# Kernel optimization log

Hardware: AMD Instinct MI355X
Metric: run time of the kernel (lower is better)

The kernel has to match this reference:

```python
import jax, jax.numpy as jnp
import numpy as np

B, M = 2048, 128

def _linear_params(key, out_dim, in_dim):
    k1, k2 = jax.random.split(key)
    bound = 1.0 / np.sqrt(in_dim)
    w = jax.random.uniform(k1, (out_dim, in_dim), jnp.float32, -bound, bound)
    b = jax.random.uniform(k2, (out_dim,), jnp.float32, -bound, bound)
    return w, b

def setup_inputs() -> dict:
    key = jax.random.key(0)
    ks = jax.random.split(key, 11)
    dyn = jax.random.normal(ks[0], (B, M, 3), jnp.float32)
    static = jax.random.normal(ks[1], (B, 3), jnp.float32)
    phi_w1, phi_b1 = _linear_params(ks[2], 120, 3)
    phi_w2, phi_b2 = _linear_params(ks[3], 100, 120)
    phi_w3, phi_b3 = _linear_params(ks[4], 80, 100)
    rho_w1, rho_b1 = _linear_params(ks[5], 60, 80)
    rho_w2, rho_b2 = _linear_params(ks[6], 60, 60)
    rho_w3, rho_b3 = _linear_params(ks[7], 40, 60)
    q_w1, q_b1 = _linear_params(ks[8], 200, 43)
    q_w2, q_b2 = _linear_params(ks[9], 100, 200)
    q_w3, q_b3 = _linear_params(ks[10], 3, 100)
    return dict(dyn=dyn, static=static,
                phi_w1=phi_w1, phi_b1=phi_b1, phi_w2=phi_w2, phi_b2=phi_b2,
                phi_w3=phi_w3, phi_b3=phi_b3,
                rho_w1=rho_w1, rho_b1=rho_b1, rho_w2=rho_w2, rho_b2=rho_b2,
                rho_w3=rho_w3, rho_b3=rho_b3,
                q_w1=q_w1, q_b1=q_b1, q_w2=q_w2, q_b2=q_b2, q_w3=q_w3, q_b3=q_b3)

def reference(dyn, static,
              phi_w1, phi_b1, phi_w2, phi_b2, phi_w3, phi_b3,
              rho_w1, rho_b1, rho_w2, rho_b2, rho_w3, rho_b3,
              q_w1, q_b1, q_w2, q_b2, q_w3, q_b3):
    relu = jax.nn.relu
    # Phi: per-element 3-layer MLP (all layers ReLU), then sum-pool over elements.
    h = relu(jnp.einsum('bmi,oi->bmo', dyn, phi_w1) + phi_b1)   # [B,M,120]
    h = relu(jnp.einsum('bmi,oi->bmo', h, phi_w2) + phi_b2)     # [B,M,100]
    h = relu(jnp.einsum('bmi,oi->bmo', h, phi_w3) + phi_b3)     # [B,M,80]
    pooled = h.sum(axis=1)                                       # [B,80] segment-sum
    # Rho: 80 -> 40 (no activation on last layer)
    r = relu(pooled @ rho_w1.T + rho_b1)
    r = relu(r @ rho_w2.T + rho_b2)
    r = r @ rho_w3.T + rho_b3                                    # [B,40]
    x = jnp.concatenate([r, static], axis=1)                     # [B,43]
    # Q head: 43 -> 3 with softmax
    q = relu(x @ q_w1.T + q_b1)
    q = relu(q @ q_w2.T + q_b2)
    q = q @ q_w3.T + q_b3
    return jax.nn.softmax(q, axis=1)                             # [B,3]
```

## Files before the change

### kernel.cpp

```cpp
#include <hip/hip_runtime.h>
#include <math.h>

typedef short s16x8 __attribute__((ext_vector_type(8)));
typedef short s16x4 __attribute__((ext_vector_type(4)));
typedef float f32x4 __attribute__((ext_vector_type(4)));

__device__ __forceinline__ void bsplit(float x, short& hi, short& lo) {
    unsigned u  = __float_as_uint(x);
    unsigned uh = u & 0xFFFF0000u;
    hi = (short)(uh >> 16);
    float r = x - __uint_as_float(uh);
    lo = (short)(__float_as_uint(r) >> 16);
}

#define MFMA_B16(A, B, C) __builtin_amdgcn_mfma_f32_16x16x32_bf16((A), (B), (C), 0, 0, 0)

__global__ __launch_bounds__(512, 4)
void ds_all(const float* __restrict__ dyn, const float* __restrict__ stat,
            const float* __restrict__ pw1, const float* __restrict__ pb1,
            const float* __restrict__ pw2, const float* __restrict__ pb2,
            const float* __restrict__ pw3, const float* __restrict__ pb3,
            const float* __restrict__ rw1, const float* __restrict__ rb1,
            const float* __restrict__ rw2, const float* __restrict__ rb2,
            const float* __restrict__ rw3, const float* __restrict__ rb3,
            const float* __restrict__ qw1, const float* __restrict__ qb1,
            const float* __restrict__ qw2, const float* __restrict__ qb2,
            const float* __restrict__ qw3, const float* __restrict__ qb3,
            float* __restrict__ out) {
    const int tid = threadIdx.x;
    const int w = tid >> 6, l = tid & 63, ln = l & 15, l4 = l >> 4;
    const int b = blockIdx.x;

    __shared__ __align__(16) float xs[384];
    __shared__ short h1H[2048], h1L[2048];
    __shared__ short h2H[2048], h2L[2048];
    __shared__ __align__(16) float pooledS[80];
    __shared__ __align__(16) float r1s[64], r2s[64], xcat[48], q1s[200], q2s[104];
    __shared__ float logits[3];

    if (tid < 96)
        *(f32x4*)(xs + tid * 4) = *(const f32x4*)(dyn + (size_t)b * 384 + tid * 4);

    if (tid < 128) {
        const int t = tid & 63, row = t >> 2, q = t & 3;
        const int col = (112 + q * 4) ^ ((row & 7) << 3);
        s16x4 z = 0;
        short* dst = (tid < 64) ? h2H : h2L;
        *(s16x4*)(dst + row * 128 + col) = z;
    }

    const int grow = tid >> 5;
    const int k0   = (tid & 31) * 4;
    f32x4 c1_0, c1_1, c1_2, c1_3;
    #define LDC(J, C) do { const int k = k0 + (J);                              \
        if (k < 120) { C.x = pw1[k*3]; C.y = pw1[k*3+1]; C.z = pw1[k*3+2];      \
                       C.w = pb1[k]; }                                          \
        else C = 0.f; } while (0)
    LDC(0, c1_0); LDC(1, c1_1); LDC(2, c1_2); LDC(3, c1_3);
    #undef LDC

    const int arow = 16 * w + ln;
    s16x8 w2h0=0,w2h1=0,w2h2=0,w2h3=0, w2l0=0,w2l1=0,w2l2=0,w2l3=0;
    s16x8 w3h0=0,w3h1=0,w3h2=0,w3h3=0, w3l0=0,w3l1=0,w3l2=0,w3l3=0;
    f32x4 bb2 = 0.f, bb3 = 0.f;
    if (w < 7) {
        #define LDW2(KS, DH, DL) do { s16x8 vh, vl;                             \
            _Pragma("unroll")                                                   \
            for (int j = 0; j < 8; ++j) {                                       \
                const int c = (KS) * 32 + l4 * 8 + j;                           \
                float v = (arow < 100 && c < 120) ? pw2[arow * 120 + c] : 0.f;  \
                short hi, lo; bsplit(v, hi, lo); vh[j] = hi; vl[j] = lo;        \
            } DH = vh; DL = vl; } while (0)
        LDW2(0, w2h0, w2l0); LDW2(1, w2h1, w2l1);
        LDW2(2, w2h2, w2l2); LDW2(3, w2h3, w2l3);
        #undef LDW2
        const int o0 = 16 * w + 4 * l4;
        #pragma unroll
        for (int r = 0; r < 4; ++r) bb2[r] = (o0 + r < 100) ? pb2[o0 + r] : 0.f;
    }
    if (w < 5) {
        #define LDW3(KS, DH, DL) do { s16x8 vh, vl;                             \
            _Pragma("unroll")                                                   \
            for (int j = 0; j < 8; ++j) {                                       \
                const int c = (KS) * 32 + l4 * 8 + j;                           \
                float v = (c < 100) ? pw3[arow * 100 + c] : 0.f;                \
                short hi, lo; bsplit(v, hi, lo); vh[j] = hi; vl[j] = lo;        \
            } DH = vh; DL = vl; } while (0)
        LDW3(0, w3h0, w3l0); LDW3(1, w3h1, w3l1);
        LDW3(2, w3h2, w3l2); LDW3(3, w3h3, w3l3);
        #undef LDW3
        bb3 = *(const f32x4*)(pb3 + 16 * w + 4 * l4);
    }
    __syncthreads();

    float pool0 = 0.f, pool1 = 0.f, pool2 = 0.f, pool3 = 0.f;
    const int swzR = (ln & 7) << 3;
    const int swzG = (grow & 7) << 3;

    #pragma unroll 1
    for (int T = 0; T < 8; ++T) {
        {
            const int el = 16 * T + grow;
            const float x0 = xs[el * 3], x1 = xs[el * 3 + 1], x2 = xs[el * 3 + 2];
            s16x4 vh, vl;
            #define GEN(J, C) do {                                              \
                float v = fmaf(x0, C.x, fmaf(x1, C.y, fmaf(x2, C.z, C.w)));     \
                v = fmaxf(v, 0.f);                                              \
                short hi, lo; bsplit(v, hi, lo); vh[J] = hi; vl[J] = lo;        \
            } while (0)
            GEN(0, c1_0); GEN(1, c1_1); GEN(2, c1_2); GEN(3, c1_3);
            #undef GEN
            const int idx = grow * 128 + (k0 ^ swzG);
            *(s16x4*)(h1H + idx) = vh;
            *(s16x4*)(h1L + idx) = vl;
        }
        __syncthreads();

        if (w < 7) {
            f32x4 a2h = 0.f, a2x = 0.f;
            #define L2K(KS, WH, WL) do {                                        \
                const int bidx = ln * 128 + (((KS) * 32 + l4 * 8) ^ swzR);      \
                const s16x8 bh = *(const s16x8*)(h1H + bidx);                   \
                const s16x8 bl = *(const s16x8*)(h1L + bidx);                   \
                a2h = MFMA_B16(WH, bh, a2h);                                    \
                a2x = MFMA_B16(WH, bl, a2x);                                    \
                a2x = MFMA_B16(WL, bh, a2x);                                    \
            } while (0)
            L2K(0, w2h0, w2l0); L2K(1, w2h1, w2l1);
            L2K(2, w2h2, w2l2); L2K(3, w2h3, w2l3);
            #undef L2K
            s16x4 oh, ol;
            #pragma unroll
            for (int r = 0; r < 4; ++r) {
                float v = fmaxf(a2h[r] + a2x[r] + bb2[r], 0.f);
                short hi, lo; bsplit(v, hi, lo);
                oh[r] = hi; ol[r] = lo;
            }
            const int idx2 = ln * 128 + ((16 * w + 4 * l4) ^ swzR);
            *(s16x4*)(h2H + idx2) = oh;
            *(s16x4*)(h2L + idx2) = ol;
        }
        __syncthreads();

        if (w < 5) {
            f32x4 a3 = 0.f, a3x = 0.f;
            #define L3K(KS, WH, WL) do {                                        \
                const int bidx = ln * 128 + (((KS) * 32 + l4 * 8) ^ swzR);      \
                const s16x8 bh = *(const s16x8*)(h2H + bidx);                   \
                const s16x8 bl = *(const s16x8*)(h2L + bidx);                   \
                a3  = MFMA_B16(WH, bh, a3);                                     \
                a3x = MFMA_B16(WH, bl, a3x);                                    \
                a3x = MFMA_B16(WL, bh, a3x);                                    \
            } while (0)
            L3K(0, w3h0, w3l0); L3K(1, w3h1, w3l1);
            L3K(2, w3h2, w3l2); L3K(3, w3h3, w3l3);
            #undef L3K
            pool0 += fmaxf(a3[0] + a3x[0] + bb3[0], 0.f);
            pool1 += fmaxf(a3[1] + a3x[1] + bb3[1], 0.f);
            pool2 += fmaxf(a3[2] + a3x[2] + bb3[2], 0.f);
            pool3 += fmaxf(a3[3] + a3x[3] + bb3[3], 0.f);
        }
        __syncthreads();
    }

    if (w < 5) {
        #pragma unroll
        for (int d = 1; d < 16; d <<= 1) {
            pool0 += __shfl_xor(pool0, d);
            pool1 += __shfl_xor(pool1, d);
            pool2 += __shfl_xor(pool2, d);
            pool3 += __shfl_xor(pool3, d);
        }
        if (ln == 0) {
            const int o0 = 16 * w + 4 * l4;
            pooledS[o0 + 0] = pool0;
            pooledS[o0 + 1] = pool1;
            pooledS[o0 + 2] = pool2;
            pooledS[o0 + 3] = pool3;
        }
    }
    __syncthreads();

    if (tid < 60) {
        float a = rb1[tid];
        for (int k = 0; k < 80; k += 4) {
            f32x4 pv = *(const f32x4*)(pooledS + k);
            f32x4 wv = *(const f32x4*)(rw1 + tid * 80 + k);
            a += pv.x * wv.x + pv.y * wv.y + pv.z * wv.z + pv.w * wv.w;
        }
        r1s[tid] = fmaxf(a, 0.0f);
    }
    __syncthreads();
    if (tid < 60) {
        float a = rb2[tid];
        for (int k = 0; k < 60; k += 4) {
            f32x4 pv = *(const f32x4*)(r1s + k);
            f32x4 wv = *(const f32x4*)(rw2 + tid * 60 + k);
            a += pv.x * wv.x + pv.y * wv.y + pv.z * wv.z + pv.w * wv.w;
        }
        r2s[tid] = fmaxf(a, 0.0f);
    }
    __syncthreads();
    if (tid < 40) {
        float a = rb3[tid];
        for (int k = 0; k < 60; k += 4) {
            f32x4 pv = *(const f32x4*)(r2s + k);
            f32x4 wv = *(const f32x4*)(rw3 + tid * 60 + k);
            a += pv.x * wv.x + pv.y * wv.y + pv.z * wv.z + pv.w * wv.w;
        }
        xcat[tid] = a;
    }
    if (tid >= 40 && tid < 43) xcat[tid] = stat[(size_t)b * 3 + (tid - 40)];
    __syncthreads();
    if (tid < 200) {
        float a = qb1[tid];
        const float* wv = qw1 + tid * 43;
        for (int k = 0; k < 43; ++k) a += xcat[k] * wv[k];
        q1s[tid] = fmaxf(a, 0.0f);
    }
    __syncthreads();
    if (tid < 100) {
        float a = qb2[tid];
        for (int k = 0; k < 200; k += 4) {
            f32x4 pv = *(const f32x4*)(q1s + k);
            f32x4 wv = *(const f32x4*)(qw2 + tid * 200 + k);
            a += pv.x * wv.x + pv.y * wv.y + pv.z * wv.z + pv.w * wv.w;
        }
        q2s[tid] = fmaxf(a, 0.0f);
    }
    __syncthreads();
    if (tid < 96) {
        int o = tid >> 5, l2 = tid & 31;
        float a = 0.0f;
        for (int k = l2; k < 100; k += 32) a += q2s[k] * qw3[o * 100 + k];
        #pragma unroll
        for (int d = 16; d > 0; d >>= 1) a += __shfl_down(a, d, 32);
        if (l2 == 0) logits[o] = a + qb3[o];
    }
    __syncthreads();
    if (tid < 3) {
        float l0 = logits[0], l1 = logits[1], l2v = logits[2];
        float m  = fmaxf(l0, fmaxf(l1, l2v));
        float e0 = __expf(l0 - m), e1 = __expf(l1 - m), e2 = __expf(l2v - m);
        float inv = 1.0f / (e0 + e1 + e2);
        float mine = (tid == 0) ? e0 : ((tid == 1) ? e1 : e2);
        out[(size_t)b * 3 + tid] = mine * inv;
    }
}

extern "C" void kernel_launch(void* const* d_in, const int* in_sizes, int n_in,
                              void* d_out, int out_size, void* d_ws, size_t ws_size,
                              hipStream_t stream) {
    const float* dyn  = (const float*)d_in[0];
    const float* stat = (const float*)d_in[1];
    const float* pw1  = (const float*)d_in[2];
    const float* pb1  = (const float*)d_in[3];
    const float* pw2  = (const float*)d_in[4];
    const float* pb2  = (const float*)d_in[5];
    const float* pw3  = (const float*)d_in[6];
    const float* pb3  = (const float*)d_in[7];
    const float* rw1  = (const float*)d_in[8];
    const float* rb1  = (const float*)d_in[9];
    const float* rw2  = (const float*)d_in[10];
    const float* rb2  = (const float*)d_in[11];
    const float* rw3  = (const float*)d_in[12];
    const float* rb3  = (const float*)d_in[13];
    const float* qw1  = (const float*)d_in[14];
    const float* qb1  = (const float*)d_in[15];
    const float* qw2  = (const float*)d_in[16];
    const float* qb2  = (const float*)d_in[17];
    const float* qw3  = (const float*)d_in[18];
    const float* qb3  = (const float*)d_in[19];
    float* out = (float*)d_out;

    const int B = in_sizes[0] / 384;
    ds_all<<<dim3(B), dim3(512), 0, stream>>>(dyn, stat,
        pw1, pb1, pw2, pb2, pw3, pb3,
        rw1, rb1, rw2, rb2, rw3, rb3,
        qw1, qb1, qw2, qb2, qw3, qb3, out);
}
```

Before: 190.6 us.

## Split MFMA accumulator chains, raise priority, and parallelize the rho/Q head dot-products

Each phi-layer MFMA sequence now uses three independent accumulators instead of two, shortening the dependent chain. Shared-memory fragment loads are batched two k-steps at a time, and the MFMA region runs at raised wave priority via s_setprio. The serial per-output dot products in the rho and Q-head tail now split each reduction across 2 or 4 lanes, combined with shuffles. The aim is less latency on the per-batch serial tail and in the MFMA chains, at the cost of extra registers and shuffle ops.

```diff
diff --git a/kernel.cpp b/kernel.cpp
--- a/kernel.cpp
+++ b/kernel.cpp
@@ -96,6 +96,7 @@
     float pool0 = 0.f, pool1 = 0.f, pool2 = 0.f, pool3 = 0.f;
     const int swzR = (ln & 7) << 3;
     const int swzG = (grow & 7) << 3;
+    #define HIDX(KS) (ln * 128 + ((((KS) * 32) + l4 * 8) ^ swzR))
 
     #pragma unroll 1
     for (int T = 0; T < 8; ++T) {
@@ -117,22 +118,37 @@
         __syncthreads();
 
         if (w < 7) {
-            f32x4 a2h = 0.f, a2x = 0.f;
-            #define L2K(KS, WH, WL) do {                                        \
-                const int bidx = ln * 128 + (((KS) * 32 + l4 * 8) ^ swzR);      \
-                const s16x8 bh = *(const s16x8*)(h1H + bidx);                   \
-                const s16x8 bl = *(const s16x8*)(h1L + bidx);                   \
-                a2h = MFMA_B16(WH, bh, a2h);                                    \
-                a2x = MFMA_B16(WH, bl, a2x);                                    \
-                a2x = MFMA_B16(WL, bh, a2x);                                    \
-            } while (0)
-            L2K(0, w2h0, w2l0); L2K(1, w2h1, w2l1);
-            L2K(2, w2h2, w2l2); L2K(3, w2h3, w2l3);
-            #undef L2K
+            f32x4 a2h = 0.f, a2x = 0.f, a2y = 0.f;
+            __builtin_amdgcn_s_setprio(1);
+            {
+                const s16x8 bh0 = *(const s16x8*)(h1H + HIDX(0));
+                const s16x8 bl0 = *(const s16x8*)(h1L + HIDX(0));
+                const s16x8 bh1v = *(const s16x8*)(h1H + HIDX(1));
+                const s16x8 bl1v = *(const s16x8*)(h1L + HIDX(1));
+                a2h = MFMA_B16(w2h0, bh0, a2h);
+                a2x = MFMA_B16(w2h0, bl0, a2x);
+                a2y = MFMA_B16(w2l0, bh0, a2y);
+                a2h = MFMA_B16(w2h1, bh1v, a2h);
+                a2x = MFMA_B16(w2h1, bl1v, a2x);
+                a2y = MFMA_B16(w2l1, bh1v, a2y);
+            }
+            {
+                const s16x8 bh2 = *(const s16x8*)(h1H + HIDX(2));
+                const s16x8 bl2 = *(const s16x8*)(h1L + HIDX(2));
+                const s16x8 bh3 = *(const s16x8*)(h1H + HIDX(3));
+                const s16x8 bl3 = *(const s16x8*)(h1L + HIDX(3));
+                a2h = MFMA_B16(w2h2, bh2, a2h);
+                a2x = MFMA_B16(w2h2, bl2, a2x);
+                a2y = MFMA_B16(w2l2, bh2, a2y);
+                a2h = MFMA_B16(w2h3, bh3, a2h);
+                a2x = MFMA_B16(w2h3, bl3, a2x);
+                a2y = MFMA_B16(w2l3, bh3, a2y);
+            }
+            __builtin_amdgcn_s_setprio(0);
             s16x4 oh, ol;
             #pragma unroll
             for (int r = 0; r < 4; ++r) {
-                float v = fmaxf(a2h[r] + a2x[r] + bb2[r], 0.f);
+                float v = fmaxf(a2h[r] + a2x[r] + a2y[r] + bb2[r], 0.f);
                 short hi, lo; bsplit(v, hi, lo);
                 oh[r] = hi; ol[r] = lo;
             }
@@ -143,25 +159,41 @@
         __syncthreads();
 
         if (w < 5) {
-            f32x4 a3 = 0.f, a3x = 0.f;
-            #define L3K(KS, WH, WL) do {                                        \
-                const int bidx = ln * 128 + (((KS) * 32 + l4 * 8) ^ swzR);      \
-                const s16x8 bh = *(const s16x8*)(h2H + bidx);                   \
-                const s16x8 bl = *(const s16x8*)(h2L + bidx);                   \
-                a3  = MFMA_B16(WH, bh, a3);                                     \
-                a3x = MFMA_B16(WH, bl, a3x);                                    \
-                a3x = MFMA_B16(WL, bh, a3x);                                    \
-            } while (0)
-            L3K(0, w3h0, w3l0); L3K(1, w3h1, w3l1);
-            L3K(2, w3h2, w3l2); L3K(3, w3h3, w3l3);
-            #undef L3K
-            pool0 += fmaxf(a3[0] + a3x[0] + bb3[0], 0.f);
-            pool1 += fmaxf(a3[1] + a3x[1] + bb3[1], 0.f);
-            pool2 += fmaxf(a3[2] + a3x[2] + bb3[2], 0.f);
-            pool3 += fmaxf(a3[3] + a3x[3] + bb3[3], 0.f);
+            f32x4 a3 = 0.f, a3x = 0.f, a3y = 0.f;
+            __builtin_amdgcn_s_setprio(1);
+            {
+                const s16x8 bh0 = *(const s16x8*)(h2H + HIDX(0));
+                const s16x8 bl0 = *(const s16x8*)(h2L + HIDX(0));
+                const s16x8 bh1v = *(const s16x8*)(h2H + HIDX(1));
+                const s16x8 bl1v = *(const s16x8*)(h2L + HIDX(1));
+                a3  = MFMA_B16(w3h0, bh0, a3);
+                a3x = MFMA_B16(w3h0, bl0, a3x);
+                a3y = MFMA_B16(w3l0, bh0, a3y);
+                a3  = MFMA_B16(w3h1, bh1v, a3);
+                a3x = MFMA_B16(w3h1, bl1v, a3x);
+                a3y = MFMA_B16(w3l1, bh1v, a3y);
+            }
+            {
+                const s16x8 bh2 = *(const s16x8*)(h2H + HIDX(2));
+                const s16x8 bl2 = *(const s16x8*)(h2L + HIDX(2));
+                const s16x8 bh3 = *(const s16x8*)(h2H + HIDX(3));
+                const s16x8 bl3 = *(const s16x8*)(h2L + HIDX(3));
+                a3  = MFMA_B16(w3h2, bh2, a3);
+                a3x = MFMA_B16(w3h2, bl2, a3x);
+                a3y = MFMA_B16(w3l2, bh2, a3y);
+                a3  = MFMA_B16(w3h3, bh3, a3);
+                a3x = MFMA_B16(w3h3, bl3, a3x);
+                a3y = MFMA_B16(w3l3, bh3, a3y);
+            }
+            __builtin_amdgcn_s_setprio(0);
+            pool0 += fmaxf(a3[0] + a3x[0] + a3y[0] + bb3[0], 0.f);
+            pool1 += fmaxf(a3[1] + a3x[1] + a3y[1] + bb3[1], 0.f);
+            pool2 += fmaxf(a3[2] + a3x[2] + a3y[2] + bb3[2], 0.f);
+            pool3 += fmaxf(a3[3] + a3x[3] + a3y[3] + bb3[3], 0.f);
         }
         __syncthreads();
     }
+    #undef HIDX
 
     if (w < 5) {
         #pragma unroll
@@ -181,52 +213,66 @@
     }
     __syncthreads();
 
-    if (tid < 60) {
-        float a = rb1[tid];
-        for (int k = 0; k < 80; k += 4) {
-            f32x4 pv = *(const f32x4*)(pooledS + k);
-            f32x4 wv = *(const f32x4*)(rw1 + tid * 80 + k);
+    if (tid < 240) {
+        const int o = tid >> 2, p = tid & 3;
+        float a = 0.f;
+        for (int c = p; c < 20; c += 4) {
+            f32x4 pv = *(const f32x4*)(pooledS + c * 4);
+            f32x4 wv = *(const f32x4*)(rw1 + o * 80 + c * 4);
             a += pv.x * wv.x + pv.y * wv.y + pv.z * wv.z + pv.w * wv.w;
         }
-        r1s[tid] = fmaxf(a, 0.0f);
-    }
-    __syncthreads();
-    if (tid < 60) {
-        float a = rb2[tid];
-        for (int k = 0; k < 60; k += 4) {
-            f32x4 pv = *(const f32x4*)(r1s + k);
-            f32x4 wv = *(const f32x4*)(rw2 + tid * 60 + k);
+        a += __shfl_xor(a, 1);
+        a += __shfl_xor(a, 2);
+        if (p == 0) r1s[o] = fmaxf(a + rb1[o], 0.f);
+    }
+    __syncthreads();
+    if (tid < 240) {
+        const int o = tid >> 2, p = tid & 3;
+        float a = 0.f;
+        for (int c = p; c < 15; c += 4) {
+            f32x4 pv = *(const f32x4*)(r1s + c * 4);
+            f32x4 wv = *(const f32x4*)(rw2 + o * 60 + c * 4);
             a += pv.x * wv.x + pv.y * wv.y + pv.z * wv.z + pv.w * wv.w;
         }
-        r2s[tid] = fmaxf(a, 0.0f);
-    }
-    __syncthreads();
-    if (tid < 40) {
-        float a = rb3[tid];
-        for (int k = 0; k < 60; k += 4) {
-            f32x4 pv = *(const f32x4*)(r2s + k);
-            f32x4 wv = *(const f32x4*)(rw3 + tid * 60 + k);
+        a += __shfl_xor(a, 1);
+        a += __shfl_xor(a, 2);
+        if (p == 0) r2s[o] = fmaxf(a + rb2[o], 0.f);
+    }
+    __syncthreads();
+    if (tid < 160) {
+        const int o = tid >> 2, p = tid & 3;
+        float a = 0.f;
+        for (int c = p; c < 15; c += 4) {
+            f32x4 pv = *(const f32x4*)(r2s + c * 4);
+            f32x4 wv = *(const f32x4*)(rw3 + o * 60 + c * 4);
             a += pv.x * wv.x + pv.y * wv.y + pv.z * wv.z + pv.w * wv.w;
         }
-        xcat[tid] = a;
-    }
-    if (tid >= 40 && tid < 43) xcat[tid] = stat[(size_t)b * 3 + (tid - 40)];
-    __syncthreads();
-    if (tid < 200) {
-        float a = qb1[tid];
-        const float* wv = qw1 + tid * 43;
-        for (int k = 0; k < 43; ++k) a += xcat[k] * wv[k];
-        q1s[tid] = fmaxf(a, 0.0f);
-    }
-    __syncthreads();
-    if (tid < 100) {
-        float a = qb2[tid];
-        for (int k = 0; k < 200; k += 4) {
-            f32x4 pv = *(const f32x4*)(q1s + k);
-            f32x4 wv = *(const f32x4*)(qw2 + tid * 200 + k);
+        a += __shfl_xor(a, 1);
+        a += __shfl_xor(a, 2);
+        if (p == 0) xcat[o] = a + rb3[o];
+    }
+    if (tid >= 160 && tid < 163) xcat[40 + tid - 160] = stat[(size_t)b * 3 + (tid - 160)];
+    __syncthreads();
+    if (tid < 400) {
+        const int o = tid >> 1, p = tid & 1;
+        float a = 0.f;
+        const float* wv = qw1 + o * 43;
+        for (int k = p; k < 43; k += 2) a += xcat[k] * wv[k];
+        a += __shfl_xor(a, 1);
+        if (p == 0) q1s[o] = fmaxf(a + qb1[o], 0.f);
+    }
+    __syncthreads();
+    if (tid < 400) {
+        const int o = tid >> 2, p = tid & 3;
+        float a = 0.f;
+        for (int c = p; c < 50; c += 4) {
+            f32x4 pv = *(const f32x4*)(q1s + c * 4);
+            f32x4 wv = *(const f32x4*)(qw2 + o * 200 + c * 4);
             a += pv.x * wv.x + pv.y * wv.y + pv.z * wv.z + pv.w * wv.w;
         }
-        q2s[tid] = fmaxf(a, 0.0f);
+        a += __shfl_xor(a, 1);
+        a += __shfl_xor(a, 2);
+        if (p == 0) q2s[o] = fmaxf(a + qb2[o], 0.f);
     }
     __syncthreads();
     if (tid < 96) {
```

Result: slower. 212.3 us (+11.4%).

## Warp-specialize phi MLP into a double-buffered three-stage pipeline

Applied to the files above, without the earlier changes.

The block grows to 1024 threads and waves are assigned fixed roles: 7 waves run layer 2, 5 waves run layer 3, and the remaining waves generate layer 1 into double-buffered LDS tiles. Each loop iteration then has a single barrier, with all three stages working on different element tiles at once, where before there were three serialized barriers per tile. Layer-1 weights are staged in LDS rather than held in registers. The cost is twice the threads per block, doubled LDS for the h1/h2 buffers, and an extra pipeline-fill iteration, which may reduce how many blocks fit on each CU.

```diff
diff --git a/kernel.cpp b/kernel.cpp
--- a/kernel.cpp
+++ b/kernel.cpp
@@ -15,7 +15,7 @@
 
 #define MFMA_B16(A, B, C) __builtin_amdgcn_mfma_f32_16x16x32_bf16((A), (B), (C), 0, 0, 0)
 
-__global__ __launch_bounds__(512, 4)
+__global__ __launch_bounds__(1024, 4)
 void ds_all(const float* __restrict__ dyn, const float* __restrict__ stat,
             const float* __restrict__ pw1, const float* __restrict__ pb1,
             const float* __restrict__ pw2, const float* __restrict__ pb2,
@@ -32,38 +32,35 @@
     const int b = blockIdx.x;
 
     __shared__ __align__(16) float xs[384];
-    __shared__ short h1H[2048], h1L[2048];
-    __shared__ short h2H[2048], h2L[2048];
+    __shared__ __align__(16) float sw1[512];
+    __shared__ short h1H[4096], h1L[4096];
+    __shared__ short h2H[4096], h2L[4096];
     __shared__ __align__(16) float pooledS[80];
     __shared__ __align__(16) float r1s[64], r2s[64], xcat[48], q1s[200], q2s[104];
     __shared__ float logits[3];
 
     if (tid < 96)
         *(f32x4*)(xs + tid * 4) = *(const f32x4*)(dyn + (size_t)b * 384 + tid * 4);
-
-    if (tid < 128) {
-        const int t = tid & 63, row = t >> 2, q = t & 3;
+    if (tid >= 128 && tid < 256) {
+        const int t = tid - 128;
+        f32x4 v = 0.f;
+        if (t < 120) { v.x = pw1[t*3]; v.y = pw1[t*3+1]; v.z = pw1[t*3+2]; v.w = pb1[t]; }
+        *(f32x4*)(sw1 + t * 4) = v;
+    }
+    if (tid >= 256 && tid < 512) {
+        const int t = tid - 256;
+        const int buf = t >> 7, hl = (t >> 6) & 1, u = t & 63;
+        const int row = u >> 2, q = u & 3;
         const int col = (112 + q * 4) ^ ((row & 7) << 3);
+        short* dst = hl ? h2L : h2H;
         s16x4 z = 0;
-        short* dst = (tid < 64) ? h2H : h2L;
-        *(s16x4*)(dst + row * 128 + col) = z;
-    }
-
-    const int grow = tid >> 5;
-    const int k0   = (tid & 31) * 4;
-    f32x4 c1_0, c1_1, c1_2, c1_3;
-    #define LDC(J, C) do { const int k = k0 + (J);                              \
-        if (k < 120) { C.x = pw1[k*3]; C.y = pw1[k*3+1]; C.z = pw1[k*3+2];      \
-                       C.w = pb1[k]; }                                          \
-        else C = 0.f; } while (0)
-    LDC(0, c1_0); LDC(1, c1_1); LDC(2, c1_2); LDC(3, c1_3);
-    #undef LDC
-
-    const int arow = 16 * w + ln;
-    s16x8 w2h0=0,w2h1=0,w2h2=0,w2h3=0, w2l0=0,w2l1=0,w2l2=0,w2l3=0;
-    s16x8 w3h0=0,w3h1=0,w3h2=0,w3h3=0, w3l0=0,w3l1=0,w3l2=0,w3l3=0;
-    f32x4 bb2 = 0.f, bb3 = 0.f;
+        *(s16x4*)(dst + buf * 2048 + row * 128 + col) = z;
+    }
+
+    s16x8 wh0=0,wh1=0,wh2=0,wh3=0, wl0=0,wl1=0,wl2=0,wl3=0;
+    f32x4 bbv = 0.f;
     if (w < 7) {
+        const int arow = 16 * w + ln;
         #define LDW2(KS, DH, DL) do { s16x8 vh, vl;                             \
             _Pragma("unroll")                                                   \
             for (int j = 0; j < 8; ++j) {                                       \
@@ -71,14 +68,14 @@
                 float v = (arow < 100 && c < 120) ? pw2[arow * 120 + c] : 0.f;  \
                 short hi, lo; bsplit(v, hi, lo); vh[j] = hi; vl[j] = lo;        \
             } DH = vh; DL = vl; } while (0)
-        LDW2(0, w2h0, w2l0); LDW2(1, w2h1, w2l1);
-        LDW2(2, w2h2, w2l2); LDW2(3, w2h3, w2l3);
+        LDW2(0, wh0, wl0); LDW2(1, wh1, wl1);
+        LDW2(2, wh2, wl2); LDW2(3, wh3, wl3);
         #undef LDW2
         const int o0 = 16 * w + 4 * l4;
         #pragma unroll
-        for (int r = 0; r < 4; ++r) bb2[r] = (o0 + r < 100) ? pb2[o0 + r] : 0.f;
-    }
-    if (w < 5) {
+        for (int r = 0; r < 4; ++r) bbv[r] = (o0 + r < 100) ? pb2[o0 + r] : 0.f;
+    } else if (w < 12) {
+        const int arow = 16 * (w - 7) + ln;
         #define LDW3(KS, DH, DL) do { s16x8 vh, vl;                             \
             _Pragma("unroll")                                                   \
             for (int j = 0; j < 8; ++j) {                                       \
@@ -86,84 +83,96 @@
                 float v = (c < 100) ? pw3[arow * 100 + c] : 0.f;                \
                 short hi, lo; bsplit(v, hi, lo); vh[j] = hi; vl[j] = lo;        \
             } DH = vh; DL = vl; } while (0)
-        LDW3(0, w3h0, w3l0); LDW3(1, w3h1, w3l1);
-        LDW3(2, w3h2, w3l2); LDW3(3, w3h3, w3l3);
+        LDW3(0, wh0, wl0); LDW3(1, wh1, wl1);
+        LDW3(2, wh2, wl2); LDW3(3, wh3, wl3);
         #undef LDW3
-        bb3 = *(const f32x4*)(pb3 + 16 * w + 4 * l4);
-    }
-    __syncthreads();
-
+        bbv = *(const f32x4*)(pb3 + 16 * (w - 7) + 4 * l4);
+    }
+    __syncthreads();
+
+    const int swzR = (ln & 7) << 3;
+    const int tg = tid & 255, grow = tg >> 4, gk0 = (tg & 15) * 8;
     float pool0 = 0.f, pool1 = 0.f, pool2 = 0.f, pool3 = 0.f;
-    const int swzR = (ln & 7) << 3;
-    const int swzG = (grow & 7) << 3;
+
+    #define GENT(TN, BUF) do {                                                  \
+        const int el = 16 * (TN) + grow;                                        \
+        const float x0 = xs[el*3], x1 = xs[el*3+1], x2 = xs[el*3+2];            \
+        s16x8 vh, vl;                                                           \
+        _Pragma("unroll")                                                       \
+        for (int j = 0; j < 8; ++j) {                                           \
+            f32x4 c = *(const f32x4*)(sw1 + (gk0 + j) * 4);                     \
+            float v = fmaf(x0, c.x, fmaf(x1, c.y, fmaf(x2, c.z, c.w)));         \
+            v = fmaxf(v, 0.f);                                                  \
+            short hi, lo; bsplit(v, hi, lo); vh[j] = hi; vl[j] = lo;            \
+        }                                                                       \
+        const int idx = (BUF) + grow * 128 + (gk0 ^ ((grow & 7) << 3));         \
+        *(s16x8*)(h1H + idx) = vh;                                              \
+        *(s16x8*)(h1L + idx) = vl;                                              \
+    } while (0)
+
+    if (w >= 12) GENT(0, 0);
+    __syncthreads();
+
+    #define L2K(BUF, KS, WH, WL) do {                                           \
+        const int bidx = (BUF) + ln * 128 + (((KS) * 32 + l4 * 8) ^ swzR);      \
+        const s16x8 bh = *(const s16x8*)(h1H + bidx);                           \
+        const s16x8 bl = *(const s16x8*)(h1L + bidx);                           \
+        a2h = MFMA_B16(WH, bh, a2h);                                            \
+        a2x = MFMA_B16(WH, bl, a2x);                                            \
+        a2x = MFMA_B16(WL, bh, a2x);                                            \
+    } while (0)
+    #define L3K(BUF, KS, WH, WL) do {                                           \
+        const int bidx = (BUF) + ln * 128 + (((KS) * 32 + l4 * 8) ^ swzR);      \
+        const s16x8 bh = *(const s16x8*)(h2H + bidx);                           \
+        const s16x8 bl = *(const s16x8*)(h2L + bidx);                           \
+        a3  = MFMA_B16(WH, bh, a3);                                             \
+        a3x = MFMA_B16(WH, bl, a3x);                                            \
+        a3x = MFMA_B16(WL, bh, a3x);                                            \
+    } while (0)
 
     #pragma unroll 1
-    for (int T = 0; T < 8; ++T) {
-        {
-            const int el = 16 * T + grow;
-            const float x0 = xs[el * 3], x1 = xs[el * 3 + 1], x2 = xs[el * 3 + 2];
-            s16x4 vh, vl;
-            #define GEN(J, C) do {                                              \
-                float v = fmaf(x0, C.x, fmaf(x1, C.y, fmaf(x2, C.z, C.w)));     \
-                v = fmaxf(v, 0.f);                                              \
-                short hi, lo; bsplit(v, hi, lo); vh[J] = hi; vl[J] = lo;        \
-            } while (0)
-            GEN(0, c1_0); GEN(1, c1_1); GEN(2, c1_2); GEN(3, c1_3);
-            #undef GEN
-            const int idx = grow * 128 + (k0 ^ swzG);
-            *(s16x4*)(h1H + idx) = vh;
-            *(s16x4*)(h1L + idx) = vl;
+    for (int T = 0; T <= 8; ++T) {
+        const int cb = (T & 1) << 11;
+        const int ob = 2048 - cb;
+        if (w >= 12) {
+            if (T < 7) {
+                const int TN = T + 1;
+                GENT(TN, ob);
+            }
+        } else if (w < 7) {
+            if (T < 8) {
+                f32x4 a2h = 0.f, a2x = 0.f;
+                L2K(cb, 0, wh0, wl0); L2K(cb, 1, wh1, wl1);
+                L2K(cb, 2, wh2, wl2); L2K(cb, 3, wh3, wl3);
+                s16x4 oh, ol;
+                #pragma unroll
+                for (int r = 0; r < 4; ++r) {
+                    float v = fmaxf(a2h[r] + a2x[r] + bbv[r], 0.f);
+                    short hi, lo; bsplit(v, hi, lo);
+                    oh[r] = hi; ol[r] = lo;
+                }
+                const int idx2 = cb + ln * 128 + ((16 * w + 4 * l4) ^ swzR);
+                *(s16x4*)(h2H + idx2) = oh;
+                *(s16x4*)(h2L + idx2) = ol;
+            }
+        } else {
+            if (T >= 1) {
+                f32x4 a3 = 0.f, a3x = 0.f;
+                L3K(ob, 0, wh0, wl0); L3K(ob, 1, wh1, wl1);
+                L3K(ob, 2, wh2, wl2); L3K(ob, 3, wh3, wl3);
+                pool0 += fmaxf(a3[0] + a3x[0] + bbv[0], 0.f);
+                pool1 += fmaxf(a3[1] + a3x[1] + bbv[1], 0.f);
+                pool2 += fmaxf(a3[2] + a3x[2] + bbv[2], 0.f);
+                pool3 += fmaxf(a3[3] + a3x[3] + bbv[3], 0.f);
+            }
         }
         __syncthreads();
-
-        if (w < 7) {
-            f32x4 a2h = 0.f, a2x = 0.f;
-            #define L2K(KS, WH, WL) do {                                        \
-                const int bidx = ln * 128 + (((KS) * 32 + l4 * 8) ^ swzR);      \
-                const s16x8 bh = *(const s16x8*)(h1H + bidx);                   \
-                const s16x8 bl = *(const s16x8*)(h1L + bidx);                   \
-                a2h = MFMA_B16(WH, bh, a2h);                                    \
-                a2x = MFMA_B16(WH, bl, a2x);                                    \
-                a2x = MFMA_B16(WL, bh, a2x);                                    \
-            } while (0)
-            L2K(0, w2h0, w2l0); L2K(1, w2h1, w2l1);
-            L2K(2, w2h2, w2l2); L2K(3, w2h3, w2l3);
-            #undef L2K
-            s16x4 oh, ol;
-            #pragma unroll
-            for (int r = 0; r < 4; ++r) {
-                float v = fmaxf(a2h[r] + a2x[r] + bb2[r], 0.f);
-                short hi, lo; bsplit(v, hi, lo);
-                oh[r] = hi; ol[r] = lo;
-            }
-            const int idx2 = ln * 128 + ((16 * w + 4 * l4) ^ swzR);
-            *(s16x4*)(h2H + idx2) = oh;
-            *(s16x4*)(h2L + idx2) = ol;
-        }
-        __syncthreads();
-
-        if (w < 5) {
-            f32x4 a3 = 0.f, a3x = 0.f;
-            #define L3K(KS, WH, WL) do {                                        \
-                const int bidx = ln * 128 + (((KS) * 32 + l4 * 8) ^ swzR);      \
-                const s16x8 bh = *(const s16x8*)(h2H + bidx);                   \
-                const s16x8 bl = *(const s16x8*)(h2L + bidx);                   \
-                a3  = MFMA_B16(WH, bh, a3);                                     \
-                a3x = MFMA_B16(WH, bl, a3x);                                    \
-                a3x = MFMA_B16(WL, bh, a3x);                                    \
-            } while (0)
-            L3K(0, w3h0, w3l0); L3K(1, w3h1, w3l1);
-            L3K(2, w3h2, w3l2); L3K(3, w3h3, w3l3);
-            #undef L3K
-            pool0 += fmaxf(a3[0] + a3x[0] + bb3[0], 0.f);
-            pool1 += fmaxf(a3[1] + a3x[1] + bb3[1], 0.f);
-            pool2 += fmaxf(a3[2] + a3x[2] + bb3[2], 0.f);
-            pool3 += fmaxf(a3[3] + a3x[3] + bb3[3], 0.f);
-        }
-        __syncthreads();
-    }
-
-    if (w < 5) {
+    }
+    #undef GENT
+    #undef L2K
+    #undef L3K
+
+    if (w >= 7 && w < 12) {
         #pragma unroll
         for (int d = 1; d < 16; d <<= 1) {
             pool0 += __shfl_xor(pool0, d);
@@ -172,7 +181,7 @@
             pool3 += __shfl_xor(pool3, d);
         }
         if (ln == 0) {
-            const int o0 = 16 * w + 4 * l4;
+            const int o0 = 16 * (w - 7) + 4 * l4;
             pooledS[o0 + 0] = pool0;
             pooledS[o0 + 1] = pool1;
             pooledS[o0 + 2] = pool2;
@@ -274,7 +283,7 @@
     float* out = (float*)d_out;
 
     const int B = in_sizes[0] / 384;
-    ds_all<<<dim3(B), dim3(512), 0, stream>>>(dyn, stat,
+    ds_all<<<dim3(B), dim3(1024), 0, stream>>>(dyn, stat,
         pw1, pb1, pw2, pb2, pw3, pb3,
         rw1, rb1, rw2, rb2, rw3, rb3,
         qw1, qb1, qw2, qb2, qw3, qb3, out);
```

Measured after the change: 251.9 us. +32.2%, slower.
